# Performance work log

Hardware: AMD Instinct MI355X
Metric: run time of the kernel (lower is better)

Reference implementation:

```python
import jax, jax.numpy as jnp
import numpy as np

IN_DIM, OUT_DIM, ATTN_DIM, N_REL = 128, 128, 64, 200
N_NODE, N_EDGE, N_QUERY = 50000, 500000, 64
VOCAB = 2 * N_REL + 1  # 401


def setup_inputs() -> dict:
    key = jax.random.key(0)
    ks = jax.random.split(key, 16)
    # edge table [E,7]: col0=r_idx, col2=rel, col4=sub, col5=obj, col6=time; cols 1,3 unused
    e = np.zeros((N_EDGE, 7), dtype=np.int64)
    e[:, 0] = np.asarray(jax.random.randint(ks[0], (N_EDGE,), 0, N_QUERY))
    e[:, 2] = np.asarray(jax.random.randint(ks[1], (N_EDGE,), 0, VOCAB))
    e[:, 4] = np.asarray(jax.random.randint(ks[2], (N_EDGE,), 0, N_NODE))
    e[:, 5] = np.asarray(jax.random.randint(ks[3], (N_EDGE,), 0, N_NODE))
    e[:, 6] = np.asarray(jax.random.randint(ks[4], (N_EDGE,), 0, 1000))
    s = 0.05
    return {
        "q_sub": jax.random.randint(ks[5], (N_QUERY,), 0, N_NODE),
        "q_rel": jax.random.randint(ks[6], (N_QUERY,), 0, VOCAB),
        "hidden": jax.random.normal(ks[7], (N_NODE, IN_DIM), jnp.float32),
        "edges": jnp.asarray(e),
        "n_node": N_NODE,
        "rela_embed": jax.random.normal(ks[8], (VOCAB, IN_DIM), jnp.float32),
        "Ws_W": jax.random.normal(ks[9], (ATTN_DIM, IN_DIM), jnp.float32) * s,
        "Wr_W": jax.random.normal(ks[10], (ATTN_DIM, IN_DIM), jnp.float32) * s,
        "Wqr_W": jax.random.normal(ks[11], (ATTN_DIM, IN_DIM), jnp.float32) * s,
        "Wqr_b": jnp.zeros((ATTN_DIM,), jnp.float32),
        "walpha_W": jax.random.normal(ks[12], (1, ATTN_DIM), jnp.float32) * s,
        "gateW_W": jax.random.normal(ks[13], (2 * IN_DIM, 3 * IN_DIM), jnp.float32) * s,
        "gateW_b": jnp.zeros((2 * IN_DIM,), jnp.float32),
        "ht_W": jax.random.normal(ks[14], (IN_DIM, 2 * IN_DIM), jnp.float32) * s,
        "ht_b": jnp.zeros((IN_DIM,), jnp.float32),
        "Wh_W": jax.random.normal(ks[15], (OUT_DIM, IN_DIM), jnp.float32) * s,
    }


def reference(q_sub, q_rel, hidden, edges, n_node, rela_embed,
              Ws_W, Wr_W, Wqr_W, Wqr_b, walpha_W,
              gateW_W, gateW_b, ht_W, ht_b, Wh_W):
    sub, rel, obj, r_idx = edges[:, 4], edges[:, 2], edges[:, 5], edges[:, 0]
    # unique+inverse on (rel,time) then embedding of rel == direct embedding lookup
    hr = rela_embed[rel]              # [E, in]
    hs = hidden[sub]                  # [E, in]
    h_qr = rela_embed[q_rel][r_idx]   # [E, in]
    # GateUnit(message=hr, factor=h_qr, hidden_state=hs)
    factors = jnp.concatenate([hr, h_qr, hs], axis=1)
    gates = jax.nn.sigmoid(factors @ gateW_W.T + gateW_b)
    update, reset = jnp.split(gates, 2, axis=1)
    cand = jnp.tanh(jnp.concatenate([hr, reset * hs], axis=1) @ ht_W.T + ht_b)
    message = (1.0 - update) * hs + update * cand
    # attention score
    pre = hs @ Ws_W.T + hr @ Wr_W.T + (h_qr @ Wqr_W.T + Wqr_b)
    alpha = jax.nn.leaky_relu(pre, 0.01) @ walpha_W.T  # [E,1]
    up_message = jax.nn.sigmoid(alpha) * message
    # scatter-sum over destination nodes + sqrt-degree normalization
    agg = jax.ops.segment_sum(up_message, obj, num_segments=n_node)
    deg = jax.ops.segment_sum(jnp.ones((up_message.shape[0], 1), jnp.float32), obj, num_segments=n_node)
    agg = agg / jnp.sqrt(deg + 0.0001)
    return agg @ Wh_W.T  # act = identity
```

## Files before the change

kernel.cpp:

```cpp
#include <hip/hip_runtime.h>

typedef unsigned short ushort_t;
typedef __attribute__((ext_vector_type(8))) short short8;
typedef __attribute__((ext_vector_type(4))) float f32x4;

#define DEV __device__ __forceinline__

DEV float sigm(float x) { return 1.0f / (1.0f + __expf(-x)); }
DEV float tanh_fast(float x) { return 1.0f - 2.0f / (__expf(2.0f * x) + 1.0f); }
DEV ushort_t f2bf(float v) {
    unsigned u = __float_as_uint(v);
    unsigned r = (u + 0x7fffu + ((u >> 16) & 1u)) >> 16;
    return (ushort_t)r;
}
DEV float bf2f(ushort_t h) { return __uint_as_float(((unsigned)h) << 16); }
DEV unsigned cvt_pk(float lo, float hi) {
    unsigned r;
    asm("v_cvt_pk_bf16_f32 %0, %1, %2" : "=v"(r) : "v"(lo), "v"(hi));
    return r;
}
DEV float dot4(float4 a, float4 b) {
    return fmaf(a.x, b.x, fmaf(a.y, b.y, fmaf(a.z, b.z, a.w * b.w)));
}

__global__ __launch_bounds__(256) void prep_kernel(
    const float* __restrict__ hidden, const float* __restrict__ gateW,
    const float* __restrict__ WsW,
    ushort_t* __restrict__ gate_hs, ushort_t* __restrict__ ws_hs,
    ushort_t* __restrict__ hsb, int nNode,
    const float* __restrict__ rela, const int* __restrict__ q_rel,
    const float* __restrict__ gateW_b,
    const float* __restrict__ WrW, const float* __restrict__ WqrW,
    const float* __restrict__ Wqr_b, const float* __restrict__ htW,
    const float* __restrict__ ht_b,
    float* __restrict__ grhr, float* __restrict__ gq,
    float* __restrict__ whr, float* __restrict__ wq,
    float* __restrict__ thr, int vocab,
    const int* __restrict__ edges, int nEdge, int* __restrict__ cnt,
    int nodeB, int tableB)
{
    __shared__ char smem[8192];
    int bid = blockIdx.x, t = threadIdx.x;

    if (bid < nodeB) {
        char* a_lds = smem;
        int w = t >> 6, l = t & 63;
        int lm = l & 15, lh = l >> 4;
        int nbase = bid * 32;

        for (int idx = t; idx < 1024; idx += 256) {
            int row = idx >> 5, c4 = idx & 31;
            int node = nbase + row;
            float4 v = (node < nNode) ? ((const float4*)hidden)[(size_t)node * 32 + c4]
                                      : float4{0.f, 0.f, 0.f, 0.f};
            uint2 p;
            p.x = cvt_pk(v.x, v.y);
            p.y = cvt_pk(v.z, v.w);
            *(uint2*)(a_lds + ((row * 256 + c4 * 8) ^ ((row & 7) << 4))) = p;
            if (node < nNode) *(uint2*)(hsb + (size_t)node * 128 + c4 * 4) = p;
        }

        short8 bfr[5][4];
#pragma unroll
        for (int nt = 0; nt < 5; nt++)
#pragma unroll
            for (int kt = 0; kt < 4; kt++) {
                int row = w * 80 + nt * 16 + lm;
                const float* src = (row < 256)
                    ? gateW + (size_t)row * 384 + 256 + kt * 32 + lh * 8
                    : WsW + (size_t)(row - 256) * 128 + kt * 32 + lh * 8;
                float4 f0 = *(const float4*)src;
                float4 f1 = *(const float4*)(src + 4);
                union { unsigned u[4]; short8 s; } tmp;
                tmp.u[0] = cvt_pk(f0.x, f0.y); tmp.u[1] = cvt_pk(f0.z, f0.w);
                tmp.u[2] = cvt_pk(f1.x, f1.y); tmp.u[3] = cvt_pk(f1.z, f1.w);
                bfr[nt][kt] = tmp.s;
            }
        __syncthreads();

        short8 afr[2][4];
#pragma unroll
        for (int mt = 0; mt < 2; mt++)
#pragma unroll
            for (int kt = 0; kt < 4; kt++) {
                int row = mt * 16 + lm;
                afr[mt][kt] = *(const short8*)(a_lds +
                    ((row * 256 + kt * 64 + lh * 16) ^ ((row & 7) << 4)));
            }
        f32x4 acc[2][5];
#pragma unroll
        for (int mt = 0; mt < 2; mt++)
#pragma unroll
            for (int nt = 0; nt < 5; nt++) acc[mt][nt] = (f32x4){0.f, 0.f, 0.f, 0.f};
#pragma unroll
        for (int kt = 0; kt < 4; kt++)
#pragma unroll
            for (int mt = 0; mt < 2; mt++)
#pragma unroll
                for (int nt = 0; nt < 5; nt++)
                    acc[mt][nt] = __builtin_amdgcn_mfma_f32_16x16x32_bf16(
                        afr[mt][kt], bfr[nt][kt], acc[mt][nt], 0, 0, 0);

#pragma unroll
        for (int mt = 0; mt < 2; mt++)
#pragma unroll
            for (int nt = 0; nt < 5; nt++) {
                int wrow = w * 80 + nt * 16 + lm;
#pragma unroll
                for (int r = 0; r < 4; r++) {
                    int node = nbase + mt * 16 + lh * 4 + r;
                    if (node < nNode) {
                        ushort_t v = f2bf(acc[mt][nt][r]);
                        if (wrow < 256)
                            gate_hs[(size_t)node * 256 + 2 * (wrow & 127) + (wrow >> 7)] = v;
                        else
                            ws_hs[(size_t)node * 64 + wrow - 256] = v;
                    }
                }
            }
    } else if (bid < nodeB + tableB) {
        float* x = (float*)smem;
        int b = bid - nodeB;
        bool isRel = b < vocab;
        int src = isRel ? b : q_rel[b - vocab];
        if (t < 128) x[t] = rela[src * 128 + t];
        __syncthreads();
        const float4* x4 = (const float4*)x;
        {
            const float4* wrow = (const float4*)(gateW + t * 384 + (isRel ? 0 : 128));
            float acc = isRel ? 0.0f : gateW_b[t];
#pragma unroll 8
            for (int i = 0; i < 32; i++) acc += dot4(wrow[i], x4[i]);
            float* dst = isRel ? (grhr + b * 256) : (gq + (b - vocab) * 256);
            dst[2 * (t & 127) + (t >> 7)] = acc;
        }
        if (isRel) {
            if (t < 192) {
                bool isWr = t < 64;
                int i = isWr ? t : (t - 64);
                const float4* wrow = (const float4*)(isWr ? (WrW + i * 128) : (htW + i * 256));
                float acc = isWr ? 0.0f : ht_b[i];
#pragma unroll 8
                for (int q = 0; q < 32; q++) acc += dot4(wrow[q], x4[q]);
                if (isWr) whr[b * 64 + i] = acc;
                else      thr[b * 128 + i] = acc;
            }
        } else {
            if (t < 64) {
                const float4* wrow = (const float4*)(WqrW + t * 128);
                float acc = Wqr_b[t];
#pragma unroll 8
                for (int q = 0; q < 32; q++) acc += dot4(wrow[q], x4[q]);
                wq[(b - vocab) * 64 + t] = acc;
            }
        }
    } else {
        int i = (bid - nodeB - tableB) * 256 + t;
        if (i < nEdge) atomicAdd(cnt + edges[(size_t)i * 7 + 5], 1);
    }
}

__global__ __launch_bounds__(256) void scan1_kernel(
    const int* __restrict__ cnt, int n, int* __restrict__ partials)
{
    __shared__ int s[256];
    int t = threadIdx.x;
    int i = blockIdx.x * 256 + t;
    s[t] = (i < n) ? cnt[i] : 0;
    __syncthreads();
    for (int o = 128; o > 0; o >>= 1) {
        if (t < o) s[t] += s[t + o];
        __syncthreads();
    }
    if (t == 0) partials[blockIdx.x] = s[0];
}

__global__ __launch_bounds__(256) void scan2_kernel(
    const int* __restrict__ cnt, int n, const int* __restrict__ partials,
    int nBlk, int* __restrict__ start, int* __restrict__ cursor)
{
    __shared__ int ps[256];
    __shared__ int loc[256];
    int t = threadIdx.x, b = blockIdx.x;
    ps[t] = (t < nBlk) ? partials[t] : 0;
    __syncthreads();
    for (int o = 1; o < 256; o <<= 1) {
        int v = (t >= o) ? ps[t - o] : 0;
        __syncthreads();
        ps[t] += v;
        __syncthreads();
    }
    int offset = (b > 0) ? ps[b - 1] : 0;
    int i = b * 256 + t;
    int v = (i < n) ? cnt[i] : 0;
    loc[t] = v;
    __syncthreads();
    for (int o = 1; o < 256; o <<= 1) {
        int x = (t >= o) ? loc[t - o] : 0;
        __syncthreads();
        loc[t] += x;
        __syncthreads();
    }
    if (i < n) {
        int excl = offset + loc[t] - v;
        start[i] = excl;
        cursor[i] = excl;
    }
}

__global__ __launch_bounds__(256) void build_kernel(
    const int* __restrict__ edges, int nEdge, int* __restrict__ cursor,
    int4* __restrict__ sorted)
{
    int i = blockIdx.x * 256 + threadIdx.x;
    if (i < nEdge) {
        const int* er = edges + (size_t)i * 7;
        int obj = er[5];
        int s = atomicAdd(cursor + obj, 1);
        sorted[s] = make_int4(er[0], er[2], er[4], obj);
    }
}

__global__ __launch_bounds__(256, 6) void edge_kernel(
    const int4* __restrict__ sorted, int nEdge,
    const float* __restrict__ grhr, const float* __restrict__ gq,
    const float* __restrict__ whr, const float* __restrict__ wq,
    const float* __restrict__ thr,
    const ushort_t* __restrict__ gate_hs, const ushort_t* __restrict__ ws_hs,
    const ushort_t* __restrict__ hsb,
    const float* __restrict__ walpha, const float* __restrict__ htW,
    float* __restrict__ agg)
{
    __shared__ ushort_t xb[32 * 128];
    __shared__ unsigned ab[32 * 128];
    __shared__ float sgaL[32];
    __shared__ int4 eds4[32];

    int t = threadIdx.x, w = t >> 6, l = t & 63;
    int lm = l & 15, lh = l >> 4;
    int n0 = w * 32;

    int nb = gridDim.x;
    int xcd = blockIdx.x & 7, lid = blockIdx.x >> 3;
    int q = nb >> 3, rr = nb & 7;
    int sbid = ((xcd < rr) ? xcd * (q + 1) : rr * (q + 1) + (xcd - rr) * q) + lid;
    int ebase = sbid * 32;

    if (t < 32) {
        int gi = ebase + t;
        eds4[t] = (gi < nEdge) ? sorted[gi] : make_int4(0, 0, 0, -1);
    }

    short8 bfr[2][4];
#pragma unroll
    for (int nt = 0; nt < 2; nt++)
#pragma unroll
        for (int kt = 0; kt < 4; kt++) {
            const float* src = htW + (size_t)(n0 + nt * 16 + lm) * 256 + 128 + kt * 32 + lh * 8;
            float4 f0 = *(const float4*)src;
            float4 f1 = *(const float4*)(src + 4);
            union { unsigned u[4]; short8 s; } tmp;
            tmp.u[0] = cvt_pk(f0.x, f0.y); tmp.u[1] = cvt_pk(f0.z, f0.w);
            tmp.u[2] = cvt_pk(f1.x, f1.y); tmp.u[3] = cvt_pk(f1.z, f1.w);
            bfr[nt][kt] = tmp.s;
        }
    float wal = walpha[l];
    __syncthreads();

    float aa8[8];
#pragma unroll
    for (int i = 0; i < 8; i++) {
        int e = w * 8 + i;
        int4 er = eds4[e];
        int ridx = er.x, rel = er.y, sub = er.z;
        ushort4 gp = *(const ushort4*)(gate_hs + (size_t)sub * 256 + 4 * l);
        float4 ga = *(const float4*)(grhr + (size_t)rel * 256 + 4 * l);
        float4 gb = *(const float4*)(gq + (size_t)ridx * 256 + 4 * l);
        unsigned hp = *(const unsigned*)(hsb + (size_t)sub * 128 + 2 * l);
        float aw = bf2f(ws_hs[(size_t)sub * 64 + l]) + whr[rel * 64 + l] + wq[ridx * 64 + l];
        float h0 = bf2f((ushort_t)(hp & 0xffffu));
        float h1 = bf2f((ushort_t)(hp >> 16));
        float u0 = sigm(ga.x + gb.x + bf2f(gp.x));
        float r0 = sigm(ga.y + gb.y + bf2f(gp.y));
        float u1 = sigm(ga.z + gb.z + bf2f(gp.z));
        float r1 = sigm(ga.w + gb.w + bf2f(gp.w));
        *(unsigned*)((char*)xb + ((e * 256 + 4 * l) ^ ((e & 7) << 4))) = cvt_pk(r0 * h0, r1 * h1);
        uint2 abp;
        abp.x = cvt_pk((1.0f - u0) * h0, u0);
        abp.y = cvt_pk((1.0f - u1) * h1, u1);
        *(uint2*)((char*)ab + ((e * 512 + 8 * l) ^ (((e >> 2) & 3) << 6))) = abp;
        aw = (aw > 0.0f) ? aw : 0.01f * aw;
        aa8[i] = aw * wal;
    }

    f32x4 acc[2][2];
#pragma unroll
    for (int mt = 0; mt < 2; mt++)
#pragma unroll
        for (int nt = 0; nt < 2; nt++) {
            int d = n0 + nt * 16 + lm;
#pragma unroll
            for (int r = 0; r < 4; r++) {
                int rel = eds4[mt * 16 + lh * 4 + r].y;
                acc[mt][nt][r] = thr[rel * 128 + d];
            }
        }

#pragma unroll
    for (int o = 32; o > 0; o >>= 1) {
#pragma unroll
        for (int i = 0; i < 8; i++) aa8[i] += __shfl_xor(aa8[i], o, 64);
    }
#pragma unroll
    for (int i = 0; i < 8; i++) {
        float s = sigm(aa8[i]);
        if (l == i) sgaL[w * 8 + i] = s;
    }
    __syncthreads();

    short8 afr[2][4];
#pragma unroll
    for (int mt = 0; mt < 2; mt++)
#pragma unroll
        for (int kt = 0; kt < 4; kt++) {
            int e = mt * 16 + lm;
            afr[mt][kt] = *(const short8*)((const char*)xb +
                ((e * 256 + kt * 64 + lh * 16) ^ ((e & 7) << 4)));
        }
#pragma unroll
    for (int kt = 0; kt < 4; kt++)
#pragma unroll
        for (int mt = 0; mt < 2; mt++)
#pragma unroll
            for (int nt = 0; nt < 2; nt++)
                acc[mt][nt] = __builtin_amdgcn_mfma_f32_16x16x32_bf16(
                    afr[mt][kt], bfr[nt][kt], acc[mt][nt], 0, 0, 0);

#pragma unroll
    for (int mt = 0; mt < 2; mt++)
#pragma unroll
        for (int nt = 0; nt < 2; nt++) {
            int d = n0 + nt * 16 + lm;
            float vals[4];
            int objs[4];
#pragma unroll
            for (int r = 0; r < 4; r++) {
                int e = mt * 16 + lh * 4 + r;
                objs[r] = eds4[e].w;
                float cand = tanh_fast(acc[mt][nt][r]);
                unsigned abw = *(const unsigned*)((const char*)ab +
                    ((e * 512 + 4 * d) ^ (((e >> 2) & 3) << 6)));
                float sg = sgaL[e];
                vals[r] = sg * (bf2f((ushort_t)(abw & 0xffffu)) +
                                bf2f((ushort_t)(abw >> 16)) * cand);
            }
            float sum = vals[0];
            int prev = objs[0];
#pragma unroll
            for (int r = 1; r < 4; r++) {
                if (objs[r] == prev) {
                    sum += vals[r];
                } else {
                    if (prev >= 0) atomicAdd(agg + (size_t)prev * 128 + d, sum);
                    sum = vals[r];
                    prev = objs[r];
                }
            }
            if (prev >= 0) atomicAdd(agg + (size_t)prev * 128 + d, sum);
        }
}

__global__ __launch_bounds__(256) void final_kernel(
    const float* __restrict__ WhW, const int* __restrict__ degi,
    float* __restrict__ agg, int nNode)
{
    __shared__ char y_lds[64 * 256];
    int t = threadIdx.x, w = t >> 6, l = t & 63;
    int lm = l & 15, lh = l >> 4;
    int nbase = blockIdx.x * 64;

    short8 bfr[2][4];
#pragma unroll
    for (int nt = 0; nt < 2; nt++)
#pragma unroll
        for (int kt = 0; kt < 4; kt++) {
            const float* src = WhW + (size_t)(w * 32 + nt * 16 + lm) * 128 + kt * 32 + lh * 8;
            float4 f0 = *(const float4*)src;
            float4 f1 = *(const float4*)(src + 4);
            union { unsigned u[4]; short8 s; } tmp;
            tmp.u[0] = cvt_pk(f0.x, f0.y); tmp.u[1] = cvt_pk(f0.z, f0.w);
            tmp.u[2] = cvt_pk(f1.x, f1.y); tmp.u[3] = cvt_pk(f1.z, f1.w);
            bfr[nt][kt] = tmp.s;
        }

    for (int idx = t; idx < 2048; idx += 256) {
        int row = idx >> 5, c4 = idx & 31;
        int node = nbase + row;
        uint2 p = {0u, 0u};
        if (node < nNode) {
            float4 v = ((const float4*)agg)[(size_t)node * 32 + c4];
            float r = 1.0f / sqrtf((float)degi[node] + 1e-4f);
            p.x = cvt_pk(v.x * r, v.y * r);
            p.y = cvt_pk(v.z * r, v.w * r);
        }
        *(uint2*)(y_lds + ((row * 256 + c4 * 8) ^ ((row & 7) << 4))) = p;
    }
    __syncthreads();

    short8 afr[4][4];
#pragma unroll
    for (int mt = 0; mt < 4; mt++)
#pragma unroll
        for (int kt = 0; kt < 4; kt++) {
            int row = mt * 16 + lm;
            afr[mt][kt] = *(const short8*)(y_lds +
                ((row * 256 + kt * 64 + lh * 16) ^ ((row & 7) << 4)));
        }
    f32x4 acc[4][2];
#pragma unroll
    for (int mt = 0; mt < 4; mt++)
#pragma unroll
        for (int nt = 0; nt < 2; nt++) acc[mt][nt] = (f32x4){0.f, 0.f, 0.f, 0.f};
#pragma unroll
    for (int kt = 0; kt < 4; kt++)
#pragma unroll
        for (int mt = 0; mt < 4; mt++)
#pragma unroll
            for (int nt = 0; nt < 2; nt++)
                acc[mt][nt] = __builtin_amdgcn_mfma_f32_16x16x32_bf16(
                    afr[mt][kt], bfr[nt][kt], acc[mt][nt], 0, 0, 0);

#pragma unroll
    for (int mt = 0; mt < 4; mt++)
#pragma unroll
        for (int nt = 0; nt < 2; nt++) {
            int col = w * 32 + nt * 16 + lm;
#pragma unroll
            for (int r = 0; r < 4; r++) {
                int node = nbase + mt * 16 + lh * 4 + r;
                if (node < nNode) agg[(size_t)node * 128 + col] = acc[mt][nt][r];
            }
        }
}

extern "C" void kernel_launch(void* const* d_in, const int* in_sizes, int n_in,
                              void* d_out, int out_size, void* d_ws, size_t ws_size,
                              hipStream_t stream)
{
    const int*   q_rel   = (const int*)d_in[1];
    const float* hidden  = (const float*)d_in[2];
    const int*   edges   = (const int*)d_in[3];
    const float* rela    = (const float*)d_in[5];
    const float* WsW     = (const float*)d_in[6];
    const float* WrW     = (const float*)d_in[7];
    const float* WqrW    = (const float*)d_in[8];
    const float* Wqr_b   = (const float*)d_in[9];
    const float* walpha  = (const float*)d_in[10];
    const float* gateW   = (const float*)d_in[11];
    const float* gateW_b = (const float*)d_in[12];
    const float* htW     = (const float*)d_in[13];
    const float* ht_b    = (const float*)d_in[14];
    const float* WhW     = (const float*)d_in[15];

    int nNode  = in_sizes[2] / 128;
    int nEdge  = in_sizes[3] / 7;
    int vocab  = in_sizes[5] / 128;
    int nQuery = in_sizes[1];

    char* ws = (char*)d_ws;
    size_t off = 0;
    auto alloc = [&](size_t bytes) { size_t o = off; off += (bytes + 255) & ~(size_t)255; return o; };
    int*      cntO    = (int*)(ws + alloc((size_t)(nNode + 256) * 4));
    int*      startO  = (int*)(ws + alloc((size_t)(nNode + 256) * 4));
    int*      cursorO = (int*)(ws + alloc((size_t)(nNode + 256) * 4));
    int*      partials= (int*)(ws + alloc(256 * 4));
    int4*     sorted  = (int4*)(ws + alloc((size_t)nEdge * 16));
    float*    grhr    = (float*)(ws + alloc((size_t)vocab * 256 * 4));
    float*    whr     = (float*)(ws + alloc((size_t)vocab * 64 * 4));
    float*    thr     = (float*)(ws + alloc((size_t)vocab * 128 * 4));
    float*    gq      = (float*)(ws + alloc((size_t)nQuery * 256 * 4));
    float*    wq      = (float*)(ws + alloc((size_t)nQuery * 64 * 4));
    ushort_t* gate_hs = (ushort_t*)(ws + alloc((size_t)nNode * 256 * 2));
    ushort_t* ws_hs   = (ushort_t*)(ws + alloc((size_t)nNode * 64 * 2));
    ushort_t* hsb     = (ushort_t*)(ws + alloc((size_t)nNode * 128 * 2));
    if (off > ws_size) return;

    float* agg = (float*)d_out;
    hipMemsetAsync(agg, 0, (size_t)nNode * 128 * 4, stream);
    hipMemsetAsync(cntO, 0, (size_t)(nNode + 256) * 4, stream);

    int nodeB  = (nNode + 31) / 32;
    int tableB = vocab + nQuery;
    int histB  = (nEdge + 255) / 256;
    prep_kernel<<<nodeB + tableB + histB, 256, 0, stream>>>(
        hidden, gateW, WsW, gate_hs, ws_hs, hsb, nNode,
        rela, q_rel, gateW_b, WrW, WqrW, Wqr_b, htW, ht_b,
        grhr, gq, whr, wq, thr, vocab,
        edges, nEdge, cntO, nodeB, tableB);

    int nScan = nNode + 1;
    int nBlk = (nScan + 255) / 256;
    scan1_kernel<<<nBlk, 256, 0, stream>>>(cntO, nScan, partials);
    scan2_kernel<<<nBlk, 256, 0, stream>>>(cntO, nScan, partials, nBlk, startO, cursorO);
    build_kernel<<<(nEdge + 255) / 256, 256, 0, stream>>>(edges, nEdge, cursorO, sorted);

    int eblocks = (nEdge + 31) / 32;
    edge_kernel<<<eblocks, 256, 0, stream>>>(
        sorted, nEdge, grhr, gq, whr, wq, thr,
        gate_hs, ws_hs, hsb, walpha, htW, agg);

    int fblocks = (nNode + 63) / 64;
    final_kernel<<<fblocks, 256, 0, stream>>>(WhW, cntO, agg, nNode);
}
```

Measured before the change: 375.6 us.

## Pack per-node/per-relation tables and make edge kernel persistent with prefetch

Merges the separate per-node bf16 tables (gate projection, Ws projection, hidden) into one 512-element row per node, and likewise packs the per-relation and per-query float tables into single strided rows. Each edge gather then reads from one contiguous row instead of several scattered arrays. The edge kernel becomes a persistent grid of 1024 blocks of 512 threads. Each block loops over batches of 32 edges, with each wave owning 16 output columns, and double-buffers the next batch's edge records. The unused start array is dropped. The risks are lower parallelism per batch, extra barriers per loop iteration, and larger padded rows that could waste cache.

```diff
diff --git a/kernel.cpp b/kernel.cpp
--- a/kernel.cpp
+++ b/kernel.cpp
@@ -23,19 +23,17 @@
     return fmaf(a.x, b.x, fmaf(a.y, b.y, fmaf(a.z, b.z, a.w * b.w)));
 }
 
+
 __global__ __launch_bounds__(256) void prep_kernel(
     const float* __restrict__ hidden, const float* __restrict__ gateW,
     const float* __restrict__ WsW,
-    ushort_t* __restrict__ gate_hs, ushort_t* __restrict__ ws_hs,
-    ushort_t* __restrict__ hsb, int nNode,
+    ushort_t* __restrict__ subtab, int nNode,
     const float* __restrict__ rela, const int* __restrict__ q_rel,
     const float* __restrict__ gateW_b,
     const float* __restrict__ WrW, const float* __restrict__ WqrW,
     const float* __restrict__ Wqr_b, const float* __restrict__ htW,
     const float* __restrict__ ht_b,
-    float* __restrict__ grhr, float* __restrict__ gq,
-    float* __restrict__ whr, float* __restrict__ wq,
-    float* __restrict__ thr, int vocab,
+    float* __restrict__ reltab, float* __restrict__ qtab, int vocab,
     const int* __restrict__ edges, int nEdge, int* __restrict__ cnt,
     int nodeB, int tableB)
 {
@@ -57,7 +55,8 @@
             p.x = cvt_pk(v.x, v.y);
             p.y = cvt_pk(v.z, v.w);
             *(uint2*)(a_lds + ((row * 256 + c4 * 8) ^ ((row & 7) << 4))) = p;
-            if (node < nNode) *(uint2*)(hsb + (size_t)node * 128 + c4 * 4) = p;
+            if (node < nNode)
+                *(uint2*)(subtab + (size_t)node * 512 + 256 + c4 * 4) = p;
         }
 
         short8 bfr[5][4];
@@ -112,9 +111,9 @@
                     if (node < nNode) {
                         ushort_t v = f2bf(acc[mt][nt][r]);
                         if (wrow < 256)
-                            gate_hs[(size_t)node * 256 + 2 * (wrow & 127) + (wrow >> 7)] = v;
+                            subtab[(size_t)node * 512 + 2 * (wrow & 127) + (wrow >> 7)] = v;
                         else
-                            ws_hs[(size_t)node * 64 + wrow - 256] = v;
+                            subtab[(size_t)node * 512 + 384 + (wrow - 256)] = v;
                     }
                 }
             }
@@ -131,19 +130,21 @@
             float acc = isRel ? 0.0f : gateW_b[t];
 #pragma unroll 8
             for (int i = 0; i < 32; i++) acc += dot4(wrow[i], x4[i]);
-            float* dst = isRel ? (grhr + b * 256) : (gq + (b - vocab) * 256);
+            float* dst = isRel ? (reltab + (size_t)b * 512)
+                               : (qtab + (size_t)(b - vocab) * 512);
             dst[2 * (t & 127) + (t >> 7)] = acc;
         }
         if (isRel) {
             if (t < 192) {
                 bool isWr = t < 64;
                 int i = isWr ? t : (t - 64);
-                const float4* wrow = (const float4*)(isWr ? (WrW + i * 128) : (htW + i * 256));
+                const float* wp = isWr ? (WrW + i * 128) : (htW + i * 256);
+                const float4* wrow = (const float4*)wp;
                 float acc = isWr ? 0.0f : ht_b[i];
 #pragma unroll 8
                 for (int q = 0; q < 32; q++) acc += dot4(wrow[q], x4[q]);
-                if (isWr) whr[b * 64 + i] = acc;
-                else      thr[b * 128 + i] = acc;
+                if (isWr) reltab[(size_t)b * 512 + 256 + i] = acc;
+                else      reltab[(size_t)b * 512 + 320 + i] = acc;
             }
         } else {
             if (t < 64) {
@@ -151,7 +152,7 @@
                 float acc = Wqr_b[t];
 #pragma unroll 8
                 for (int q = 0; q < 32; q++) acc += dot4(wrow[q], x4[q]);
-                wq[(b - vocab) * 64 + t] = acc;
+                qtab[(size_t)(b - vocab) * 512 + 256 + t] = acc;
             }
         }
     } else {
@@ -177,7 +178,7 @@
 
 __global__ __launch_bounds__(256) void scan2_kernel(
     const int* __restrict__ cnt, int n, const int* __restrict__ partials,
-    int nBlk, int* __restrict__ start, int* __restrict__ cursor)
+    int nBlk, int* __restrict__ cursor)
 {
     __shared__ int ps[256];
     __shared__ int loc[256];
@@ -201,11 +202,7 @@
         loc[t] += x;
         __syncthreads();
     }
-    if (i < n) {
-        int excl = offset + loc[t] - v;
-        start[i] = excl;
-        cursor[i] = excl;
-    }
+    if (i < n) cursor[i] = offset + loc[t] - v;
 }
 
 __global__ __launch_bounds__(256) void build_kernel(
@@ -221,138 +218,132 @@
     }
 }
 
-__global__ __launch_bounds__(256, 6) void edge_kernel(
-    const int4* __restrict__ sorted, int nEdge,
-    const float* __restrict__ grhr, const float* __restrict__ gq,
-    const float* __restrict__ whr, const float* __restrict__ wq,
-    const float* __restrict__ thr,
-    const ushort_t* __restrict__ gate_hs, const ushort_t* __restrict__ ws_hs,
-    const ushort_t* __restrict__ hsb,
+__global__ __launch_bounds__(512, 6) void edge_kernel(
+    const int4* __restrict__ sorted, int nEdge, int nBatch, int K,
+    const float* __restrict__ reltab, const float* __restrict__ qtab,
+    const ushort_t* __restrict__ subtab,
     const float* __restrict__ walpha, const float* __restrict__ htW,
     float* __restrict__ agg)
 {
     __shared__ ushort_t xb[32 * 128];
     __shared__ unsigned ab[32 * 128];
     __shared__ float sgaL[32];
-    __shared__ int4 eds4[32];
+    __shared__ int4 eds4[2][32];
 
     int t = threadIdx.x, w = t >> 6, l = t & 63;
     int lm = l & 15, lh = l >> 4;
-    int n0 = w * 32;
+    int n0 = w * 16;
 
     int nb = gridDim.x;
     int xcd = blockIdx.x & 7, lid = blockIdx.x >> 3;
-    int q = nb >> 3, rr = nb & 7;
-    int sbid = ((xcd < rr) ? xcd * (q + 1) : rr * (q + 1) + (xcd - rr) * q) + lid;
-    int ebase = sbid * 32;
+    int qq = nb >> 3, rr = nb & 7;
+    int sbid = ((xcd < rr) ? xcd * (qq + 1) : rr * (qq + 1) + (xcd - rr) * qq) + lid;
+    int b0 = sbid * K;
+    int b1 = min(b0 + K, nBatch);
+    if (b0 >= nBatch) return;
+
+    short8 bfr[4];
+#pragma unroll
+    for (int kt = 0; kt < 4; kt++) {
+        const float* src = htW + (size_t)(n0 + lm) * 256 + 128 + kt * 32 + lh * 8;
+        float4 f0 = *(const float4*)src;
+        float4 f1 = *(const float4*)(src + 4);
+        union { unsigned u[4]; short8 s; } tmp;
+        tmp.u[0] = cvt_pk(f0.x, f0.y); tmp.u[1] = cvt_pk(f0.z, f0.w);
+        tmp.u[2] = cvt_pk(f1.x, f1.y); tmp.u[3] = cvt_pk(f1.z, f1.w);
+        bfr[kt] = tmp.s;
+    }
+    float wal = walpha[l];
 
     if (t < 32) {
-        int gi = ebase + t;
-        eds4[t] = (gi < nEdge) ? sorted[gi] : make_int4(0, 0, 0, -1);
-    }
-
-    short8 bfr[2][4];
-#pragma unroll
-    for (int nt = 0; nt < 2; nt++)
-#pragma unroll
-        for (int kt = 0; kt < 4; kt++) {
-            const float* src = htW + (size_t)(n0 + nt * 16 + lm) * 256 + 128 + kt * 32 + lh * 8;
-            float4 f0 = *(const float4*)src;
-            float4 f1 = *(const float4*)(src + 4);
-            union { unsigned u[4]; short8 s; } tmp;
-            tmp.u[0] = cvt_pk(f0.x, f0.y); tmp.u[1] = cvt_pk(f0.z, f0.w);
-            tmp.u[2] = cvt_pk(f1.x, f1.y); tmp.u[3] = cvt_pk(f1.z, f1.w);
-            bfr[nt][kt] = tmp.s;
-        }
-    float wal = walpha[l];
+        int gi = b0 * 32 + t;
+        eds4[0][t] = (gi < nEdge) ? sorted[gi] : make_int4(0, 0, 0, -1);
+    }
     __syncthreads();
 
-    float aa8[8];
-#pragma unroll
-    for (int i = 0; i < 8; i++) {
-        int e = w * 8 + i;
-        int4 er = eds4[e];
-        int ridx = er.x, rel = er.y, sub = er.z;
-        ushort4 gp = *(const ushort4*)(gate_hs + (size_t)sub * 256 + 4 * l);
-        float4 ga = *(const float4*)(grhr + (size_t)rel * 256 + 4 * l);
-        float4 gb = *(const float4*)(gq + (size_t)ridx * 256 + 4 * l);
-        unsigned hp = *(const unsigned*)(hsb + (size_t)sub * 128 + 2 * l);
-        float aw = bf2f(ws_hs[(size_t)sub * 64 + l]) + whr[rel * 64 + l] + wq[ridx * 64 + l];
-        float h0 = bf2f((ushort_t)(hp & 0xffffu));
-        float h1 = bf2f((ushort_t)(hp >> 16));
-        float u0 = sigm(ga.x + gb.x + bf2f(gp.x));
-        float r0 = sigm(ga.y + gb.y + bf2f(gp.y));
-        float u1 = sigm(ga.z + gb.z + bf2f(gp.z));
-        float r1 = sigm(ga.w + gb.w + bf2f(gp.w));
-        *(unsigned*)((char*)xb + ((e * 256 + 4 * l) ^ ((e & 7) << 4))) = cvt_pk(r0 * h0, r1 * h1);
-        uint2 abp;
-        abp.x = cvt_pk((1.0f - u0) * h0, u0);
-        abp.y = cvt_pk((1.0f - u1) * h1, u1);
-        *(uint2*)((char*)ab + ((e * 512 + 8 * l) ^ (((e >> 2) & 3) << 6))) = abp;
-        aw = (aw > 0.0f) ? aw : 0.01f * aw;
-        aa8[i] = aw * wal;
-    }
-
-    f32x4 acc[2][2];
-#pragma unroll
-    for (int mt = 0; mt < 2; mt++)
-#pragma unroll
-        for (int nt = 0; nt < 2; nt++) {
-            int d = n0 + nt * 16 + lm;
+    int cur = 0;
+    for (int b = b0; b < b1; ++b) {
+        float aa4[4];
+#pragma unroll
+        for (int i = 0; i < 4; i++) {
+            int e = w * 4 + i;
+            int4 er = eds4[cur][e];
+            int ridx = er.x, rel = er.y, sub = er.z;
+            const ushort_t* sb = subtab + (size_t)sub * 512;
+            const float* rb = reltab + (size_t)rel * 512;
+            const float* qb = qtab + (size_t)ridx * 512;
+            ushort4 gp = *(const ushort4*)(sb + 4 * l);
+            float4 ga = *(const float4*)(rb + 4 * l);
+            float4 gb4 = *(const float4*)(qb + 4 * l);
+            unsigned hp = *(const unsigned*)(sb + 256 + 2 * l);
+            float aw = bf2f(sb[384 + l]) + rb[256 + l] + qb[256 + l];
+            float h0 = bf2f((ushort_t)(hp & 0xffffu));
+            float h1 = bf2f((ushort_t)(hp >> 16));
+            float u0 = sigm(ga.x + gb4.x + bf2f(gp.x));
+            float r0 = sigm(ga.y + gb4.y + bf2f(gp.y));
+            float u1 = sigm(ga.z + gb4.z + bf2f(gp.z));
+            float r1 = sigm(ga.w + gb4.w + bf2f(gp.w));
+            *(unsigned*)((char*)xb + ((e * 256 + 4 * l) ^ ((e & 7) << 4))) =
+                cvt_pk(r0 * h0, r1 * h1);
+            uint2 abp;
+            abp.x = cvt_pk((1.0f - u0) * h0, u0);
+            abp.y = cvt_pk((1.0f - u1) * h1, u1);
+            *(uint2*)((char*)ab + ((e * 512 + 8 * l) ^ (((e >> 2) & 3) << 6))) = abp;
+            aa4[i] = fmaxf(aw, 0.01f * aw) * wal;
+        }
+
+        f32x4 acc[2];
+#pragma unroll
+        for (int mt = 0; mt < 2; mt++)
 #pragma unroll
             for (int r = 0; r < 4; r++) {
-                int rel = eds4[mt * 16 + lh * 4 + r].y;
-                acc[mt][nt][r] = thr[rel * 128 + d];
-            }
-        }
-
-#pragma unroll
-    for (int o = 32; o > 0; o >>= 1) {
-#pragma unroll
-        for (int i = 0; i < 8; i++) aa8[i] += __shfl_xor(aa8[i], o, 64);
-    }
-#pragma unroll
-    for (int i = 0; i < 8; i++) {
-        float s = sigm(aa8[i]);
-        if (l == i) sgaL[w * 8 + i] = s;
-    }
-    __syncthreads();
-
-    short8 afr[2][4];
-#pragma unroll
-    for (int mt = 0; mt < 2; mt++)
-#pragma unroll
-        for (int kt = 0; kt < 4; kt++) {
-            int e = mt * 16 + lm;
-            afr[mt][kt] = *(const short8*)((const char*)xb +
-                ((e * 256 + kt * 64 + lh * 16) ^ ((e & 7) << 4)));
-        }
-#pragma unroll
-    for (int kt = 0; kt < 4; kt++)
-#pragma unroll
-        for (int mt = 0; mt < 2; mt++)
-#pragma unroll
-            for (int nt = 0; nt < 2; nt++)
-                acc[mt][nt] = __builtin_amdgcn_mfma_f32_16x16x32_bf16(
-                    afr[mt][kt], bfr[nt][kt], acc[mt][nt], 0, 0, 0);
-
-#pragma unroll
-    for (int mt = 0; mt < 2; mt++)
-#pragma unroll
-        for (int nt = 0; nt < 2; nt++) {
-            int d = n0 + nt * 16 + lm;
+                int rel = eds4[cur][mt * 16 + lh * 4 + r].y;
+                acc[mt][r] = reltab[(size_t)rel * 512 + 320 + n0 + lm];
+            }
+
+#pragma unroll
+        for (int o = 32; o > 0; o >>= 1)
+#pragma unroll
+            for (int i = 0; i < 4; i++) aa4[i] += __shfl_xor(aa4[i], o, 64);
+#pragma unroll
+        for (int i = 0; i < 4; i++)
+            if (l == i) sgaL[w * 4 + i] = sigm(aa4[i]);
+
+        if (b + 1 < b1 && t < 32) {
+            int gi = (b + 1) * 32 + t;
+            eds4[cur ^ 1][t] = (gi < nEdge) ? sorted[gi] : make_int4(0, 0, 0, -1);
+        }
+        __syncthreads();
+
+#pragma unroll
+        for (int mt = 0; mt < 2; mt++) {
+            short8 afr[4];
+#pragma unroll
+            for (int kt = 0; kt < 4; kt++) {
+                int e = mt * 16 + lm;
+                afr[kt] = *(const short8*)((const char*)xb +
+                    ((e * 256 + kt * 64 + lh * 16) ^ ((e & 7) << 4)));
+            }
+#pragma unroll
+            for (int kt = 0; kt < 4; kt++)
+                acc[mt] = __builtin_amdgcn_mfma_f32_16x16x32_bf16(
+                    afr[kt], bfr[kt], acc[mt], 0, 0, 0);
+        }
+
+        int d = n0 + lm;
+#pragma unroll
+        for (int mt = 0; mt < 2; mt++) {
             float vals[4];
             int objs[4];
 #pragma unroll
             for (int r = 0; r < 4; r++) {
                 int e = mt * 16 + lh * 4 + r;
-                objs[r] = eds4[e].w;
-                float cand = tanh_fast(acc[mt][nt][r]);
+                objs[r] = eds4[cur][e].w;
+                float cand = tanh_fast(acc[mt][r]);
                 unsigned abw = *(const unsigned*)((const char*)ab +
                     ((e * 512 + 4 * d) ^ (((e >> 2) & 3) << 6)));
-                float sg = sgaL[e];
-                vals[r] = sg * (bf2f((ushort_t)(abw & 0xffffu)) +
-                                bf2f((ushort_t)(abw >> 16)) * cand);
+                vals[r] = sgaL[e] * (bf2f((ushort_t)(abw & 0xffffu)) +
+                                     bf2f((ushort_t)(abw >> 16)) * cand);
             }
             float sum = vals[0];
             int prev = objs[0];
@@ -368,6 +359,9 @@
             }
             if (prev >= 0) atomicAdd(agg + (size_t)prev * 128 + d, sum);
         }
+        __syncthreads();
+        cur ^= 1;
+    }
 }
 
 __global__ __launch_bounds__(256) void final_kernel(
@@ -471,18 +465,12 @@
     size_t off = 0;
     auto alloc = [&](size_t bytes) { size_t o = off; off += (bytes + 255) & ~(size_t)255; return o; };
     int*      cntO    = (int*)(ws + alloc((size_t)(nNode + 256) * 4));
-    int*      startO  = (int*)(ws + alloc((size_t)(nNode + 256) * 4));
     int*      cursorO = (int*)(ws + alloc((size_t)(nNode + 256) * 4));
     int*      partials= (int*)(ws + alloc(256 * 4));
     int4*     sorted  = (int4*)(ws + alloc((size_t)nEdge * 16));
-    float*    grhr    = (float*)(ws + alloc((size_t)vocab * 256 * 4));
-    float*    whr     = (float*)(ws + alloc((size_t)vocab * 64 * 4));
-    float*    thr     = (float*)(ws + alloc((size_t)vocab * 128 * 4));
-    float*    gq      = (float*)(ws + alloc((size_t)nQuery * 256 * 4));
-    float*    wq      = (float*)(ws + alloc((size_t)nQuery * 64 * 4));
-    ushort_t* gate_hs = (ushort_t*)(ws + alloc((size_t)nNode * 256 * 2));
-    ushort_t* ws_hs   = (ushort_t*)(ws + alloc((size_t)nNode * 64 * 2));
-    ushort_t* hsb     = (ushort_t*)(ws + alloc((size_t)nNode * 128 * 2));
+    float*    reltab  = (float*)(ws + alloc((size_t)vocab * 512 * 4));
+    float*    qtab    = (float*)(ws + alloc((size_t)nQuery * 512 * 4));
+    ushort_t* subtab  = (ushort_t*)(ws + alloc((size_t)nNode * 512 * 2));
     if (off > ws_size) return;
 
     float* agg = (float*)d_out;
@@ -493,21 +481,22 @@
     int tableB = vocab + nQuery;
     int histB  = (nEdge + 255) / 256;
     prep_kernel<<<nodeB + tableB + histB, 256, 0, stream>>>(
-        hidden, gateW, WsW, gate_hs, ws_hs, hsb, nNode,
+        hidden, gateW, WsW, subtab, nNode,
         rela, q_rel, gateW_b, WrW, WqrW, Wqr_b, htW, ht_b,
-        grhr, gq, whr, wq, thr, vocab,
+        reltab, qtab, vocab,
         edges, nEdge, cntO, nodeB, tableB);
 
     int nScan = nNode + 1;
     int nBlk = (nScan + 255) / 256;
     scan1_kernel<<<nBlk, 256, 0, stream>>>(cntO, nScan, partials);
-    scan2_kernel<<<nBlk, 256, 0, stream>>>(cntO, nScan, partials, nBlk, startO, cursorO);
+    scan2_kernel<<<nBlk, 256, 0, stream>>>(cntO, nScan, partials, nBlk, cursorO);
     build_kernel<<<(nEdge + 255) / 256, 256, 0, stream>>>(edges, nEdge, cursorO, sorted);
 
-    int eblocks = (nEdge + 31) / 32;
-    edge_kernel<<<eblocks, 256, 0, stream>>>(
-        sorted, nEdge, grhr, gq, whr, wq, thr,
-        gate_hs, ws_hs, hsb, walpha, htW, agg);
+    int nBatch = (nEdge + 31) / 32;
+    int GRID = nBatch < 1024 ? nBatch : 1024;
+    int K = (nBatch + GRID - 1) / GRID;
+    edge_kernel<<<GRID, 512, 0, stream>>>(
+        sorted, nEdge, nBatch, K, reltab, qtab, subtab, walpha, htW, agg);
 
     int fblocks = (nNode + 63) / 64;
     final_kernel<<<fblocks, 256, 0, stream>>>(WhW, cntO, agg, nNode);
```

After: 542.4 us. 1.44x slower.
